# Kernel optimization log

Hardware: AMD Instinct MI355X
Metric: run time of the kernel (lower is better)

Reference implementation:

```python
import jax, jax.numpy as jnp
import numpy as np

B, S = 10000, 32        # batch nodes, sampled neighbors per node
N, D_IN, D_H = 100000, 512, 512


def setup_inputs() -> dict:
    key = jax.random.key(0)
    k1, k2, k3 = jax.random.split(key, 3)
    neigh_idx = jax.random.randint(k1, (B, S), 0, N)                 # int neighbor ids
    features = jax.random.normal(k2, (N, D_IN), dtype=jnp.float32)   # node feature table
    W = jax.random.normal(k3, (D_H, D_IN), dtype=jnp.float32) * (1.0 / np.sqrt(D_IN))
    b = jnp.zeros((D_H,), dtype=jnp.float32)
    return {"neigh_idx": neigh_idx, "features": features, "W": W, "b": b}


def reference(neigh_idx, features, W, b):
    # gather neighbor embeddings: [B, S, D_IN]
    neigh_feats = features[neigh_idx]
    # MLP: Linear(input_dim, hidden_dim) + ReLU  -> [B, S, D_H]
    h = jax.nn.relu(jnp.einsum("bsd,hd->bsh", neigh_feats, W) + b)
    # mask-based mean pool over sampled neighbors (mask @ embed / row_sum) -> [B, D_H]
    return jnp.mean(h, axis=1)
```

## Files before the change

### kernel.cpp

```cpp
#include <hip/hip_runtime.h>
#include <hip/hip_bf16.h>


#define S_NB 32
#define D_IN 512
#define D_H  512
#define BM   128
#define BN   128
#define BK   64
#define NK   (D_IN / BK)
#define NNODE 100000
#define NPAD  100352
#define NBATCH 10000
#define NTILE_N 4
#define NTILE_M 784
#define NTILES  (NTILE_N * NTILE_M)

typedef __attribute__((ext_vector_type(8))) short  short8;
typedef __attribute__((ext_vector_type(4))) float  f32x4;
typedef __attribute__((ext_vector_type(4))) unsigned short us4;
typedef __attribute__((ext_vector_type(8))) unsigned short us8;

__device__ __forceinline__ unsigned short f2bf(float x) {
  union { float f; unsigned u; } v; v.f = x;
  unsigned r = v.u + 0x7FFFu + ((v.u >> 16) & 1u);
  return (unsigned short)(r >> 16);
}

__device__ __forceinline__ float bf2f(unsigned short x) {
  union { unsigned u; float f; } v; v.u = ((unsigned)x) << 16;
  return v.f;
}

__device__ __forceinline__ int swz(int row, int cb) {
  return row * 128 + (cb ^ ((row & 7) << 4));
}

__device__ __forceinline__ void gld_lds16(const void* g, void* l) {
  __builtin_amdgcn_global_load_lds(
      (const __attribute__((address_space(1))) unsigned int*)g,
      (__attribute__((address_space(3))) unsigned int*)l, 16, 0, 0);
}

__global__ __launch_bounds__(256, 8)
void cvt_bf16(const float* __restrict__ src, unsigned short* __restrict__ dst, int n8) {
  int i = blockIdx.x * blockDim.x + threadIdx.x;
  const int stride = gridDim.x * blockDim.x;
  for (; i < n8; i += stride) {
    f32x4 a = *(const f32x4*)(src + (size_t)i * 8);
    f32x4 b = *(const f32x4*)(src + (size_t)i * 8 + 4);
    us8 o;
    o[0] = f2bf(a.x); o[1] = f2bf(a.y); o[2] = f2bf(a.z); o[3] = f2bf(a.w);
    o[4] = f2bf(b.x); o[5] = f2bf(b.y); o[6] = f2bf(b.z); o[7] = f2bf(b.w);
    *(us8*)(dst + (size_t)i * 8) = o;
  }
}

__global__ __launch_bounds__(256, 4)
void gemm_hb3(const unsigned short* __restrict__ featb,
              const unsigned short* __restrict__ Wb,
              const float* __restrict__ bias,
              unsigned short* __restrict__ Hb) {
  const int tid  = threadIdx.x;
  const int lane = tid & 63;
  const int wid  = tid >> 6;
  const int wr   = wid >> 1;
  const int wc   = wid & 1;

  const int bid  = blockIdx.x;
  const int tile = (bid & 7) * (NTILES / 8) + (bid >> 3);
  const int n0   = (tile & 3) * BN;
  const int m0   = (tile >> 2) * BM;

  __shared__ __align__(16) unsigned short smem[BM * BK * 2];
  unsigned short* As = smem;
  unsigned short* Bs = smem + BM * BK;

  const int rlb = wid * 32 + (lane >> 3);
  const int g   = (lane & 7) ^ (lane >> 3);
  const unsigned short* sA = featb + (size_t)(m0 + rlb) * D_IN + g * 8;
  const unsigned short* sB = Wb    + (size_t)(n0 + rlb) * D_IN + g * 8;
  unsigned short* dA = As + (wid * 32) * 64;
  unsigned short* dB = Bs + (wid * 32) * 64;

  f32x4 acc[4][4];
#pragma unroll
  for (int i = 0; i < 4; ++i)
#pragma unroll
    for (int j = 0; j < 4; ++j)
      acc[i][j] = (f32x4){0.f, 0.f, 0.f, 0.f};

  const int frow = lane & 15;
  const int kcb  = (lane >> 4) * 16;
  const int arow = wr * 64 + frow;
  const int brow = wc * 64 + frow;

  for (int ki = 0; ki < NK; ++ki) {
    const int k0 = ki * BK;
    if (ki) __syncthreads();
#pragma unroll
    for (int i = 0; i < 4; ++i) {
      gld_lds16(sA + k0 + i * 4096, dA + i * 512);
      gld_lds16(sB + k0 + i * 4096, dB + i * 512);
    }
    __syncthreads();

#pragma unroll
    for (int kk = 0; kk < 2; ++kk) {
      short8 af[4], bfr[4];
#pragma unroll
      for (int mi = 0; mi < 4; ++mi)
        af[mi] = *(const short8*)((const char*)As + swz(arow + mi * 16, kk * 64 + kcb));
#pragma unroll
      for (int ni = 0; ni < 4; ++ni)
        bfr[ni] = *(const short8*)((const char*)Bs + swz(brow + ni * 16, kk * 64 + kcb));
#pragma unroll
      for (int mi = 0; mi < 4; ++mi)
#pragma unroll
        for (int ni = 0; ni < 4; ++ni)
          acc[mi][ni] = __builtin_amdgcn_mfma_f32_16x16x32_bf16(af[mi], bfr[ni], acc[mi][ni], 0, 0, 0);
    }
  }

  __syncthreads();
  unsigned short* Cs = smem;
  const int rq = lane >> 4;
#pragma unroll
  for (int ni = 0; ni < 4; ++ni) {
    int col = wc * 64 + ni * 16 + frow;
    float bv = bias[n0 + col];
#pragma unroll
    for (int mi = 0; mi < 4; ++mi) {
#pragma unroll
      for (int r = 0; r < 4; ++r) {
        int row = wr * 64 + mi * 16 + rq * 4 + r;
        int byt = row * 256 + ((col * 2) ^ ((row & 7) << 4));
        *(unsigned short*)((char*)Cs + byt) = f2bf(fmaxf(acc[mi][ni][r] + bv, 0.f));
      }
    }
  }
  __syncthreads();

  const int scol = (tid & 15) * 8;
#pragma unroll
  for (int it = 0; it < 8; ++it) {
    int row  = it * 16 + (tid >> 4);
    int grow = m0 + row;
    int byt  = row * 256 + (((tid & 15) * 16) ^ ((row & 7) << 4));
    us8 v = *(const us8*)((const char*)Cs + byt);
    if (grow < NNODE)
      *(us8*)(Hb + (size_t)grow * D_H + n0 + scol) = v;
  }
}

__global__ __launch_bounds__(256, 8)
void pool_mean4(const unsigned short* __restrict__ Hb,
                const int* __restrict__ nidx,
                float* __restrict__ out) {
  const int b4 = blockIdx.x;
  const int q  = threadIdx.x >> 6;
  const int t  = threadIdx.x & 63;
  const int b  = b4 * 4 + q;

  __shared__ int rows[4][S_NB];
  if (threadIdx.x < 4 * S_NB)
    rows[threadIdx.x >> 5][threadIdx.x & 31] = nidx[b4 * 4 * S_NB + threadIdx.x];
  __syncthreads();

  const int c = t * 8;
  float s0 = 0.f, s1 = 0.f, s2 = 0.f, s3 = 0.f;
  float s4 = 0.f, s5 = 0.f, s6 = 0.f, s7 = 0.f;
#pragma unroll
  for (int s = 0; s < S_NB; ++s) {
    us8 v = *(const us8*)(Hb + (size_t)rows[q][s] * D_H + c);
    s0 += bf2f(v[0]); s1 += bf2f(v[1]); s2 += bf2f(v[2]); s3 += bf2f(v[3]);
    s4 += bf2f(v[4]); s5 += bf2f(v[5]); s6 += bf2f(v[6]); s7 += bf2f(v[7]);
  }
  const float inv = 1.0f / (float)S_NB;
  f32x4 o1; o1.x = s0 * inv; o1.y = s1 * inv; o1.z = s2 * inv; o1.w = s3 * inv;
  f32x4 o2; o2.x = s4 * inv; o2.y = s5 * inv; o2.z = s6 * inv; o2.w = s7 * inv;
  *(f32x4*)(out + (size_t)b * D_H + c)     = o1;
  *(f32x4*)(out + (size_t)b * D_H + c + 4) = o2;
}

__global__ __launch_bounds__(256, 4)
void gemm_h(const float* __restrict__ feat,
            const float* __restrict__ Wm,
            const float* __restrict__ bias,
            unsigned short* __restrict__ Hb) {
  const int tid  = threadIdx.x;
  const int lane = tid & 63;
  const int wid  = tid >> 6;
  const int wr   = wid >> 1;
  const int wc   = wid & 1;
  const int n0   = blockIdx.x * BN;
  const int m0   = blockIdx.y * BM;

  __shared__ __align__(16) unsigned short As[BM * 64];
  __shared__ __align__(16) unsigned short Bs[BM * 64];

  const int lr = tid >> 4;
  const int lc = tid & 15;

  const float* aptr[8];
  const float* wptr[8];
#pragma unroll
  for (int p = 0; p < 8; ++p) {
    int row = p * 16 + lr;
    int gr  = m0 + row; if (gr > NNODE - 1) gr = NNODE - 1;
    aptr[p] = feat + (size_t)gr * D_IN + lc * 4;
    wptr[p] = Wm + (size_t)(n0 + row) * D_IN + lc * 4;
  }

  f32x4 acc[4][4];
#pragma unroll
  for (int i = 0; i < 4; ++i)
#pragma unroll
    for (int j = 0; j < 4; ++j)
      acc[i][j] = (f32x4){0.f, 0.f, 0.f, 0.f};

  const int frow = lane & 15;
  const int kcb  = (lane >> 4) * 16;
  const int arow = wr * 64 + frow;
  const int brow = wc * 64 + frow;

  for (int k0 = 0; k0 < D_IN; k0 += 64) {
    __syncthreads();
#pragma unroll
    for (int p = 0; p < 8; ++p) {
      int row = p * 16 + lr;
      f32x4 av = *(const f32x4*)(aptr[p] + k0);
      f32x4 wv = *(const f32x4*)(wptr[p] + k0);
      us4 a4, w4;
      a4.x = f2bf(av.x); a4.y = f2bf(av.y); a4.z = f2bf(av.z); a4.w = f2bf(av.w);
      w4.x = f2bf(wv.x); w4.y = f2bf(wv.y); w4.z = f2bf(wv.z); w4.w = f2bf(wv.w);
      *(us4*)((char*)As + swz(row, lc * 8)) = a4;
      *(us4*)((char*)Bs + swz(row, lc * 8)) = w4;
    }
    __syncthreads();

#pragma unroll
    for (int kk = 0; kk < 2; ++kk) {
      short8 af[4], bfr[4];
#pragma unroll
      for (int mi = 0; mi < 4; ++mi)
        af[mi] = *(const short8*)((const char*)As + swz(arow + mi * 16, kk * 64 + kcb));
#pragma unroll
      for (int ni = 0; ni < 4; ++ni)
        bfr[ni] = *(const short8*)((const char*)Bs + swz(brow + ni * 16, kk * 64 + kcb));
#pragma unroll
      for (int mi = 0; mi < 4; ++mi)
#pragma unroll
        for (int ni = 0; ni < 4; ++ni)
          acc[mi][ni] = __builtin_amdgcn_mfma_f32_16x16x32_bf16(af[mi], bfr[ni], acc[mi][ni], 0, 0, 0);
    }
  }

  const int rq = lane >> 4;
#pragma unroll
  for (int ni = 0; ni < 4; ++ni) {
    int col = n0 + wc * 64 + ni * 16 + frow;
    float bv = bias[col];
#pragma unroll
    for (int mi = 0; mi < 4; ++mi) {
#pragma unroll
      for (int r = 0; r < 4; ++r) {
        int grow = m0 + wr * 64 + mi * 16 + rq * 4 + r;
        if (grow < NNODE)
          Hb[(size_t)grow * D_H + col] = f2bf(fmaxf(acc[mi][ni][r] + bv, 0.f));
      }
    }
  }
}

__global__ __launch_bounds__(256, 4)
void pool_aggr_gemm(const int* __restrict__ nidx_g,
                    const float* __restrict__ feat,
                    const float* __restrict__ Wm,
                    const float* __restrict__ bias,
                    float* __restrict__ out) {
  const int tid  = threadIdx.x;
  const int lane = tid & 63;
  const int wid  = tid >> 6;
  const int wr   = wid >> 1;
  const int wc   = wid & 1;
  const int n0   = blockIdx.x * BN;
  const int mb   = blockIdx.y;

  __shared__ __align__(16) unsigned short As[BM * 64];
  __shared__ __align__(16) unsigned short Bs[BM * 64];
  __shared__ int nid[BM];

  if (tid < BM) nid[tid] = nidx_g[mb * BM + tid];
  __syncthreads();

  const int lr = tid >> 4;
  const int lc = tid & 15;

  const float* aptr[8];
  const float* wptr[8];
#pragma unroll
  for (int p = 0; p < 8; ++p) {
    int row = p * 16 + lr;
    aptr[p] = feat + (size_t)nid[row] * D_IN + lc * 4;
    wptr[p] = Wm + (size_t)(n0 + row) * D_IN + lc * 4;
  }

  f32x4 acc[4][4];
#pragma unroll
  for (int i = 0; i < 4; ++i)
#pragma unroll
    for (int j = 0; j < 4; ++j)
      acc[i][j] = (f32x4){0.f, 0.f, 0.f, 0.f};

  const int frow = lane & 15;
  const int kcb  = (lane >> 4) * 16;
  const int arow = wr * 64 + frow;
  const int brow = wc * 64 + frow;

  for (int k0 = 0; k0 < D_IN; k0 += 64) {
    __syncthreads();
#pragma unroll
    for (int p = 0; p < 8; ++p) {
      int row = p * 16 + lr;
      f32x4 av = *(const f32x4*)(aptr[p] + k0);
      f32x4 wv = *(const f32x4*)(wptr[p] + k0);
      us4 a4, w4;
      a4.x = f2bf(av.x); a4.y = f2bf(av.y); a4.z = f2bf(av.z); a4.w = f2bf(av.w);
      w4.x = f2bf(wv.x); w4.y = f2bf(wv.y); w4.z = f2bf(wv.z); w4.w = f2bf(wv.w);
      *(us4*)((char*)As + swz(row, lc * 8)) = a4;
      *(us4*)((char*)Bs + swz(row, lc * 8)) = w4;
    }
    __syncthreads();

#pragma unroll
    for (int kk = 0; kk < 2; ++kk) {
      short8 af[4], bfr[4];
#pragma unroll
      for (int mi = 0; mi < 4; ++mi)
        af[mi] = *(const short8*)((const char*)As + swz(arow + mi * 16, kk * 64 + kcb));
#pragma unroll
      for (int ni = 0; ni < 4; ++ni)
        bfr[ni] = *(const short8*)((const char*)Bs + swz(brow + ni * 16, kk * 64 + kcb));
#pragma unroll
      for (int mi = 0; mi < 4; ++mi)
#pragma unroll
        for (int ni = 0; ni < 4; ++ni)
          acc[mi][ni] = __builtin_amdgcn_mfma_f32_16x16x32_bf16(af[mi], bfr[ni], acc[mi][ni], 0, 0, 0);
    }
  }

  const int rq = lane >> 4;
#pragma unroll
  for (int ni = 0; ni < 4; ++ni) {
    int col = n0 + wc * 64 + ni * 16 + frow;
    float bv = bias[col];
#pragma unroll
    for (int bl = 0; bl < 2; ++bl) {
      float s = 0.f;
#pragma unroll
      for (int m2 = 0; m2 < 2; ++m2) {
        int mi = bl * 2 + m2;
#pragma unroll
        for (int r = 0; r < 4; ++r)
          s += fmaxf(acc[mi][ni][r] + bv, 0.f);
      }
      s += __shfl_xor(s, 16);
      s += __shfl_xor(s, 32);
      if (rq == 0) {
        int bb = mb * 4 + wr * 2 + bl;
        out[(size_t)bb * D_H + col] = s * (1.0f / (float)S_NB);
      }
    }
  }
}

extern "C" void kernel_launch(void* const* d_in, const int* in_sizes, int n_in,
                              void* d_out, int out_size, void* d_ws, size_t ws_size,
                              hipStream_t stream) {
  const int*   nidx = (const int*)d_in[0];
  const float* feat = (const float*)d_in[1];
  const float* Wm   = (const float*)d_in[2];
  const float* bias = (const float*)d_in[3];
  float* out = (float*)d_out;

  const size_t featb_elems = (size_t)NPAD * D_IN;
  const size_t wb_elems    = (size_t)D_H * D_IN;
  const size_t h_elems     = (size_t)NNODE * D_H;
  const size_t need = (featb_elems + wb_elems + h_elems) * sizeof(unsigned short);
  const size_t h_bytes = h_elems * sizeof(unsigned short);

  if (ws_size >= need) {
    unsigned short* featb = (unsigned short*)d_ws;
    unsigned short* Wb    = featb + featb_elems;
    unsigned short* Hb    = Wb + wb_elems;
    cvt_bf16<<<2048, 256, 0, stream>>>(feat, featb, NNODE * D_IN / 8);
    cvt_bf16<<<128, 256, 0, stream>>>(Wm, Wb, D_H * D_IN / 8);
    gemm_hb3<<<NTILES, 256, 0, stream>>>(featb, Wb, bias, Hb);
    pool_mean4<<<NBATCH / 4, 256, 0, stream>>>(Hb, nidx, out);
  } else if (ws_size >= h_bytes) {
    unsigned short* Hb = (unsigned short*)d_ws;
    dim3 g1(D_H / BN, (NNODE + 127) / 128);
    gemm_h<<<g1, 256, 0, stream>>>(feat, Wm, bias, Hb);
    pool_mean4<<<NBATCH / 4, 256, 0, stream>>>(Hb, nidx, out);
  } else {
    dim3 grid(D_H / BN, NBATCH / 4);
    pool_aggr_gemm<<<grid, 256, 0, stream>>>(nidx, feat, Wm, bias, out);
  }
}
```

Before: 186.4 us.

## Replace bf16 GEMM with 256x256-tile 8-wave double-buffered pipelined kernel

Replaces the 128x128 single-buffered GEMM over all 100k feature rows with a 256x256-tile kernel using 512 threads and 8 waves. The 128 KB LDS is split into two stages, and loads for the next K-step are issued while MFMAs run on the current one, with s_setprio used around the MFMA blocks. Larger tiles raise operand reuse and the double buffer hides global-load latency, in exchange for one block per CU and a high register count for the 8x4 accumulators. The change also removes the BM/BN macros from the fallback kernels.

```diff
diff --git a/kernel.cpp b/kernel.cpp
--- a/kernel.cpp
+++ b/kernel.cpp
@@ -5,16 +5,10 @@
 #define S_NB 32
 #define D_IN 512
 #define D_H  512
-#define BM   128
-#define BN   128
-#define BK   64
-#define NK   (D_IN / BK)
 #define NNODE 100000
 #define NPAD  100352
 #define NBATCH 10000
-#define NTILE_N 4
-#define NTILE_M 784
-#define NTILES  (NTILE_N * NTILE_M)
+#define NT8   784
 
 typedef __attribute__((ext_vector_type(8))) short  short8;
 typedef __attribute__((ext_vector_type(4))) float  f32x4;
@@ -56,100 +50,138 @@
   }
 }
 
-__global__ __launch_bounds__(256, 4)
-void gemm_hb3(const unsigned short* __restrict__ featb,
-              const unsigned short* __restrict__ Wb,
-              const float* __restrict__ bias,
-              unsigned short* __restrict__ Hb) {
+__global__ __launch_bounds__(512, 1)
+void gemm8(const unsigned short* __restrict__ featb,
+           const unsigned short* __restrict__ Wb,
+           const float* __restrict__ bias,
+           unsigned short* __restrict__ Hb) {
   const int tid  = threadIdx.x;
   const int lane = tid & 63;
-  const int wid  = tid >> 6;
-  const int wr   = wid >> 1;
-  const int wc   = wid & 1;
+  const int w    = tid >> 6;
+  const int wm   = w >> 2;
+  const int wn   = w & 3;
 
   const int bid  = blockIdx.x;
-  const int tile = (bid & 7) * (NTILES / 8) + (bid >> 3);
-  const int n0   = (tile & 3) * BN;
-  const int m0   = (tile >> 2) * BM;
-
-  __shared__ __align__(16) unsigned short smem[BM * BK * 2];
-  unsigned short* As = smem;
-  unsigned short* Bs = smem + BM * BK;
-
-  const int rlb = wid * 32 + (lane >> 3);
-  const int g   = (lane & 7) ^ (lane >> 3);
-  const unsigned short* sA = featb + (size_t)(m0 + rlb) * D_IN + g * 8;
-  const unsigned short* sB = Wb    + (size_t)(n0 + rlb) * D_IN + g * 8;
-  unsigned short* dA = As + (wid * 32) * 64;
-  unsigned short* dB = Bs + (wid * 32) * 64;
-
-  f32x4 acc[4][4];
-#pragma unroll
-  for (int i = 0; i < 4; ++i)
+  const int tile = (bid & 7) * (NT8 / 8) + (bid >> 3);
+  const int n0   = (tile & 1) * 256;
+  const int m0   = (tile >> 1) * 256;
+
+  __shared__ __align__(16) unsigned short lds8[65536];
+  char* ldsb = (char*)&lds8[0];
+
+  const int srow = w * 16 + (lane >> 3);
+  const int g    = (lane & 7) ^ (lane >> 3);
+  const unsigned short* sA = featb + (size_t)(m0 + srow) * D_IN + g * 8;
+  const unsigned short* sB = Wb    + (size_t)(n0 + srow) * D_IN + g * 8;
+
+  auto stageA = [&](int d, int q, int t) {
+    const unsigned short* s = sA + q * 65536 + t * 64;
+    unsigned short* o = &lds8[d * 16384 + q * 8192 + w * 1024];
+    gld_lds16(s,        o);
+    gld_lds16(s + 4096, o + 512);
+  };
+  auto stageB = [&](int d, int q, int t) {
+    const unsigned short* s = sB + q * 65536 + t * 64;
+    unsigned short* o = &lds8[32768 + d * 16384 + q * 8192 + w * 1024];
+    gld_lds16(s,        o);
+    gld_lds16(s + 4096, o + 512);
+  };
+
+  f32x4 acc[8][4];
+#pragma unroll
+  for (int i = 0; i < 8; ++i)
 #pragma unroll
     for (int j = 0; j < 4; ++j)
       acc[i][j] = (f32x4){0.f, 0.f, 0.f, 0.f};
 
   const int frow = lane & 15;
-  const int kcb  = (lane >> 4) * 16;
-  const int arow = wr * 64 + frow;
-  const int brow = wc * 64 + frow;
-
-  for (int ki = 0; ki < NK; ++ki) {
-    const int k0 = ki * BK;
-    if (ki) __syncthreads();
-#pragma unroll
-    for (int i = 0; i < 4; ++i) {
-      gld_lds16(sA + k0 + i * 4096, dA + i * 512);
-      gld_lds16(sB + k0 + i * 4096, dB + i * 512);
-    }
-    __syncthreads();
-
-#pragma unroll
-    for (int kk = 0; kk < 2; ++kk) {
-      short8 af[4], bfr[4];
-#pragma unroll
-      for (int mi = 0; mi < 4; ++mi)
-        af[mi] = *(const short8*)((const char*)As + swz(arow + mi * 16, kk * 64 + kcb));
-#pragma unroll
-      for (int ni = 0; ni < 4; ++ni)
-        bfr[ni] = *(const short8*)((const char*)Bs + swz(brow + ni * 16, kk * 64 + kcb));
-#pragma unroll
-      for (int mi = 0; mi < 4; ++mi)
+  const int jg   = lane >> 4;
+  const int kx0  = ((0 * 64) + jg * 16) ^ ((frow & 7) << 4);
+  const int kx1  = ((1 * 64) + jg * 16) ^ ((frow & 7) << 4);
+  const int arb  = (wm * 128 + frow) * 128;
+  const int brb  = 65536 + (wn * 64 + frow) * 128;
+
+  stageA(0, 0, 0); stageA(0, 1, 0);
+  stageB(0, 0, 0); stageB(0, 1, 0);
+  asm volatile("s_waitcnt vmcnt(0)" ::: "memory");
+  __builtin_amdgcn_s_barrier();
+  __builtin_amdgcn_sched_barrier(0);
+
+#pragma unroll
+  for (int t = 0; t < 8; ++t) {
+    const int d  = (t & 1) * 32768;
+    short8 bfr[4][2];
+#pragma unroll
+    for (int p = 0; p < 4; ++p) {
+      if (p == 0) {
+#pragma unroll
+        for (int ni = 0; ni < 4; ++ni) {
+          bfr[ni][0] = *(const short8*)(ldsb + brb + ni * 2048 + d + kx0);
+          bfr[ni][1] = *(const short8*)(ldsb + brb + ni * 2048 + d + kx1);
+        }
+      }
+      short8 af[2][2];
+#pragma unroll
+      for (int mii = 0; mii < 2; ++mii) {
+        int mi = p * 2 + mii;
+        af[mii][0] = *(const short8*)(ldsb + arb + mi * 2048 + d + kx0);
+        af[mii][1] = *(const short8*)(ldsb + arb + mi * 2048 + d + kx1);
+      }
+
+      if (t < 7) {
+        const int d1 = (t + 1) & 1;
+        if (p == 0)      { stageA(d1, 0, t + 1); stageA(d1, 1, t + 1); }
+        else if (p == 1) { stageB(d1, 0, t + 1); stageB(d1, 1, t + 1); }
+      }
+
+      asm volatile("s_waitcnt lgkmcnt(0)" ::: "memory");
+      __builtin_amdgcn_sched_barrier(0);
+
+      __builtin_amdgcn_s_setprio(1);
+#pragma unroll
+      for (int mii = 0; mii < 2; ++mii)
 #pragma unroll
         for (int ni = 0; ni < 4; ++ni)
-          acc[mi][ni] = __builtin_amdgcn_mfma_f32_16x16x32_bf16(af[mi], bfr[ni], acc[mi][ni], 0, 0, 0);
-    }
-  }
-
+#pragma unroll
+          for (int kk = 0; kk < 2; ++kk)
+            acc[p * 2 + mii][ni] =
+                __builtin_amdgcn_mfma_f32_16x16x32_bf16(af[mii][kk], bfr[ni][kk],
+                                                        acc[p * 2 + mii][ni], 0, 0, 0);
+      __builtin_amdgcn_s_setprio(0);
+
+      if (p == 3 && t < 7)
+        asm volatile("s_waitcnt vmcnt(0)" ::: "memory");
+      __builtin_amdgcn_s_barrier();
+      __builtin_amdgcn_sched_barrier(0);
+    }
+  }
+
+  unsigned short* Cs = &lds8[0];
+#pragma unroll
+  for (int ni = 0; ni < 4; ++ni) {
+    int col = wn * 64 + ni * 16 + frow;
+    float bv = bias[n0 + col];
+#pragma unroll
+    for (int mi = 0; mi < 8; ++mi) {
+#pragma unroll
+      for (int r = 0; r < 4; ++r) {
+        int row = wm * 128 + mi * 16 + jg * 4 + r;
+        int byt = row * 512 + ((col * 2) ^ ((row & 7) << 4));
+        *(unsigned short*)((char*)Cs + byt) = f2bf(fmaxf(acc[mi][ni][r] + bv, 0.f));
+      }
+    }
+  }
   __syncthreads();
-  unsigned short* Cs = smem;
-  const int rq = lane >> 4;
-#pragma unroll
-  for (int ni = 0; ni < 4; ++ni) {
-    int col = wc * 64 + ni * 16 + frow;
-    float bv = bias[n0 + col];
-#pragma unroll
-    for (int mi = 0; mi < 4; ++mi) {
-#pragma unroll
-      for (int r = 0; r < 4; ++r) {
-        int row = wr * 64 + mi * 16 + rq * 4 + r;
-        int byt = row * 256 + ((col * 2) ^ ((row & 7) << 4));
-        *(unsigned short*)((char*)Cs + byt) = f2bf(fmaxf(acc[mi][ni][r] + bv, 0.f));
-      }
-    }
-  }
-  __syncthreads();
-
-  const int scol = (tid & 15) * 8;
-#pragma unroll
-  for (int it = 0; it < 8; ++it) {
-    int row  = it * 16 + (tid >> 4);
+
+  const int scolg = tid & 31;
+#pragma unroll
+  for (int it = 0; it < 16; ++it) {
+    int row  = it * 16 + (tid >> 5);
     int grow = m0 + row;
-    int byt  = row * 256 + (((tid & 15) * 16) ^ ((row & 7) << 4));
+    int byt  = row * 512 + ((scolg * 16) ^ ((row & 7) << 4));
     us8 v = *(const us8*)((const char*)Cs + byt);
     if (grow < NNODE)
-      *(us8*)(Hb + (size_t)grow * D_H + n0 + scol) = v;
+      *(us8*)(Hb + (size_t)grow * D_H + n0 + scolg * 8) = v;
   }
 }
 
@@ -193,11 +225,11 @@
   const int wid  = tid >> 6;
   const int wr   = wid >> 1;
   const int wc   = wid & 1;
-  const int n0   = blockIdx.x * BN;
-  const int m0   = blockIdx.y * BM;
-
-  __shared__ __align__(16) unsigned short As[BM * 64];
-  __shared__ __align__(16) unsigned short Bs[BM * 64];
+  const int n0   = blockIdx.x * 128;
+  const int m0   = blockIdx.y * 128;
+
+  __shared__ __align__(16) unsigned short As[128 * 64];
+  __shared__ __align__(16) unsigned short Bs[128 * 64];
 
   const int lr = tid >> 4;
   const int lc = tid & 15;
@@ -284,14 +316,14 @@
   const int wid  = tid >> 6;
   const int wr   = wid >> 1;
   const int wc   = wid & 1;
-  const int n0   = blockIdx.x * BN;
+  const int n0   = blockIdx.x * 128;
   const int mb   = blockIdx.y;
 
-  __shared__ __align__(16) unsigned short As[BM * 64];
-  __shared__ __align__(16) unsigned short Bs[BM * 64];
-  __shared__ int nid[BM];
-
-  if (tid < BM) nid[tid] = nidx_g[mb * BM + tid];
+  __shared__ __align__(16) unsigned short As[128 * 64];
+  __shared__ __align__(16) unsigned short Bs[128 * 64];
+  __shared__ int nid[128];
+
+  if (tid < 128) nid[tid] = nidx_g[mb * 128 + tid];
   __syncthreads();
 
   const int lr = tid >> 4;
@@ -396,15 +428,15 @@
     unsigned short* Hb    = Wb + wb_elems;
     cvt_bf16<<<2048, 256, 0, stream>>>(feat, featb, NNODE * D_IN / 8);
     cvt_bf16<<<128, 256, 0, stream>>>(Wm, Wb, D_H * D_IN / 8);
-    gemm_hb3<<<NTILES, 256, 0, stream>>>(featb, Wb, bias, Hb);
+    gemm8<<<NT8, 512, 0, stream>>>(featb, Wb, bias, Hb);
     pool_mean4<<<NBATCH / 4, 256, 0, stream>>>(Hb, nidx, out);
   } else if (ws_size >= h_bytes) {
     unsigned short* Hb = (unsigned short*)d_ws;
-    dim3 g1(D_H / BN, (NNODE + 127) / 128);
+    dim3 g1(D_H / 128, (NNODE + 127) / 128);
     gemm_h<<<g1, 256, 0, stream>>>(feat, Wm, bias, Hb);
     pool_mean4<<<NBATCH / 4, 256, 0, stream>>>(Hb, nidx, out);
   } else {
-    dim3 grid(D_H / BN, NBATCH / 4);
+    dim3 grid(D_H / 128, NBATCH / 4);
     pool_aggr_gemm<<<grid, 256, 0, stream>>>(nidx, feat, Wm, bias, out);
   }
 }
```

Result: slower. 194.9 us (+4.6%).
